# Kernel tuning notes

Measured on AMD Instinct MI355X. Metric: run time of the kernel, lower is better.

Reference implementation:

```python
import jax, jax.numpy as jnp
import numpy as np
import math

B, N, E, H = 2, 10000, 160000, 128
ET = 8
EPS = 1e-5


def setup_inputs() -> dict:
    key = jax.random.key(0)
    ks = jax.random.split(key, 20)
    s = 1.0 / math.sqrt(H)
    inp = {
        "hidden": jax.random.normal(ks[0], (B, N, H), jnp.float32),
        "time_emb": jax.random.normal(ks[1], (B, N, H), jnp.float32),
        "edge_index": jax.random.randint(ks[2], (2, E), 0, N),
        "edge_type": jax.random.randint(ks[3], (E,), 0, ET),
        # parameters
        "edge_emb": jax.random.normal(ks[4], (ET, H), jnp.float32),
        "Wq": jax.random.normal(ks[5], (H, H), jnp.float32) * s,
        "bq": jnp.zeros((H,), jnp.float32),
        "Wk": jax.random.normal(ks[6], (H, H), jnp.float32) * s,
        "bk": jnp.zeros((H,), jnp.float32),
        "Wv": jax.random.normal(ks[7], (H, H), jnp.float32) * s,
        "bv": jnp.zeros((H,), jnp.float32),
        "We": jax.random.normal(ks[8], (H, 1), jnp.float32) * s,
        "be": jnp.zeros((1,), jnp.float32),
        "W1": jax.random.normal(ks[9], (3 * H, H), jnp.float32) * (1.0 / math.sqrt(3 * H)),
        "b1": jnp.zeros((H,), jnp.float32),
        "W2": jax.random.normal(ks[10], (H, H), jnp.float32) * s,
        "b2": jnp.zeros((H,), jnp.float32),
        "gamma": jnp.ones((H,), jnp.float32),
        "beta": jnp.zeros((H,), jnp.float32),
    }
    return inp


def _forward(hidden, time_emb, edge_index, edge_type, edge_emb,
             Wq, bq, Wk, bk, Wv, bv, We, be, W1, b1, W2, b2, gamma, beta):
    src, tgt = edge_index[0], edge_index[1]
    # edge-wise gathers: [B, E, H]
    src_h = hidden[:, src]
    tgt_h = hidden[:, tgt]
    src_t = time_emb[:, src]
    tgt_t = time_emb[:, tgt]
    edge_h = edge_emb[edge_type][None, :, :]  # [1, E, H] broadcasts over batch

    query = (tgt_h + tgt_t) @ Wq + bq
    key = (src_h + src_t + edge_h) @ Wk + bk
    value = (src_h + edge_h) @ Wv + bv

    logits = jnp.einsum("beh,beh->be", query, key) / math.sqrt(H)
    logits = logits + (edge_h @ We + be)[..., 0]  # edge bias broadcast over batch

    # segment softmax per target node (equivalent to the per-node masked softmax loop)
    lT = logits.T  # [E, B]
    seg_max = jax.ops.segment_max(lT, tgt, num_segments=N)          # [N, B]
    seg_max = jnp.where(jnp.isfinite(seg_max), seg_max, 0.0)
    ex = jnp.exp(lT - seg_max[tgt])                                  # [E, B]
    seg_sum = jax.ops.segment_sum(ex, tgt, num_segments=N)           # [N, B]
    weights = (ex / seg_sum[tgt]).T                                  # [B, E]

    messages = value * weights[..., None]                            # [B, E, H]
    # scatter-add to target nodes
    agg = jax.ops.segment_sum(jnp.swapaxes(messages, 0, 1), tgt, num_segments=N)  # [N, B, H]
    aggregated = jnp.swapaxes(agg, 0, 1)                             # [B, N, H]

    cat = jnp.concatenate([hidden, aggregated, time_emb], axis=-1)   # [B, N, 3H]
    updated = jax.nn.silu(cat @ W1 + b1) @ W2 + b2

    x = hidden + updated  # dropout p=0 -> identity
    mu = jnp.mean(x, axis=-1, keepdims=True)
    var = jnp.var(x, axis=-1, keepdims=True)
    return (x - mu) * jax.lax.rsqrt(var + EPS) * gamma + beta


def reference(hidden, time_emb, edge_index, edge_type, edge_emb,
              Wq, bq, Wk, bk, Wv, bv, We, be, W1, b1, W2, b2, gamma, beta):
    return _forward(hidden, time_emb, edge_index, edge_type, edge_emb,
                    Wq, bq, Wk, bk, Wv, bv, We, be, W1, b1, W2, b2, gamma, beta)
```

## Files before the change

kernel.cpp:

```cpp
#include <hip/hip_runtime.h>
#include <math.h>

constexpr int B_  = 2;
constexpr int N_  = 10000;
constexpr int E_  = 160000;
constexpr int H_  = 128;
constexpr int ET_ = 8;
constexpr float EPS_ = 1e-5f;
constexpr float RSQH = 0.08838834764831845f;

typedef __bf16 bf16x8 __attribute__((ext_vector_type(8)));
typedef short  short8 __attribute__((ext_vector_type(8)));
typedef float  f32x4  __attribute__((ext_vector_type(4)));
typedef unsigned short u16;

__device__ inline u16 bf16b(float f) {
    return __builtin_bit_cast(u16, (__bf16)f);
}

__global__ __launch_bounds__(512)
void prep_w_kernel(const float* __restrict__ W1, const float* __restrict__ W2,
                   const float* __restrict__ Wq, const float* __restrict__ Wk,
                   const float* __restrict__ Wv,
                   u16* __restrict__ W1s, u16* __restrict__ W2s,
                   u16* __restrict__ Wqs, u16* __restrict__ Wks,
                   u16* __restrict__ Wvs)
{
    int bid = blockIdx.x;
    const float* src; u16* dst; int kc;
    if (bid < 12)      { src = W1; dst = W1s; kc = bid; }
    else if (bid < 16) { src = W2; dst = W2s; kc = bid - 12; }
    else if (bid < 20) { src = Wq; dst = Wqs; kc = bid - 16; }
    else if (bid < 24) { src = Wk; dst = Wks; kc = bid - 20; }
    else               { src = Wv; dst = Wvs; kc = bid - 24; }
    int nt = threadIdx.x >> 6, lane = threadIdx.x & 63;
    int q = lane >> 4, c = lane & 15;
    int kbase = kc * 32 + q * 8;
    int col = nt * 16 + c;
    u16* out = dst + ((kc * 8 + nt) * 64 + lane) * 8;
#pragma unroll
    for (int j = 0; j < 8; ++j)
        out[j] = bf16b(src[(kbase + j) * H_ + col]);
}

__device__ inline bf16x8 ldfrag(const u16* __restrict__ W, int kc, int nt, int lane) {
    short8 s = *(const short8*)(W + ((kc * 8 + nt) * 64 + lane) * 8);
    return __builtin_bit_cast(bf16x8, s);
}

__global__ __launch_bounds__(256)
void qkv_mfma_kernel(const float* __restrict__ hidden, const float* __restrict__ time_emb,
                     const u16* __restrict__ Wqs, const u16* __restrict__ Wks,
                     const u16* __restrict__ Wvs, const float* __restrict__ bq,
                     u16* __restrict__ Q, u16* __restrict__ K, u16* __restrict__ V)
{
    const int wv = threadIdx.x >> 6, lane = threadIdx.x & 63;
    const int tile = blockIdx.x * 4 + wv;
    if (tile >= (B_ * N_) / 16) return;
    const int nbase = tile * 16;
    const int m = lane & 15, q = lane >> 4;
    const int koff = q * 8;

    bf16x8 aq[4], av[4];
    const float* hp = hidden   + (nbase + m) * H_ + koff;
    const float* tp = time_emb + (nbase + m) * H_ + koff;
#pragma unroll
    for (int kc = 0; kc < 4; ++kc) {
        float4 h0 = *(const float4*)(hp + kc * 32);
        float4 h1 = *(const float4*)(hp + kc * 32 + 4);
        float4 t0 = *(const float4*)(tp + kc * 32);
        float4 t1 = *(const float4*)(tp + kc * 32 + 4);
        bf16x8 fv, fq;
        fv[0]=(__bf16)h0.x; fv[1]=(__bf16)h0.y; fv[2]=(__bf16)h0.z; fv[3]=(__bf16)h0.w;
        fv[4]=(__bf16)h1.x; fv[5]=(__bf16)h1.y; fv[6]=(__bf16)h1.z; fv[7]=(__bf16)h1.w;
        fq[0]=(__bf16)(h0.x+t0.x); fq[1]=(__bf16)(h0.y+t0.y);
        fq[2]=(__bf16)(h0.z+t0.z); fq[3]=(__bf16)(h0.w+t0.w);
        fq[4]=(__bf16)(h1.x+t1.x); fq[5]=(__bf16)(h1.y+t1.y);
        fq[6]=(__bf16)(h1.z+t1.z); fq[7]=(__bf16)(h1.w+t1.w);
        av[kc] = fv; aq[kc] = fq;
    }

    f32x4 accq[8], acck[8], accv[8];
#pragma unroll
    for (int nt = 0; nt < 8; ++nt) { accq[nt] = (f32x4)0.f; acck[nt] = (f32x4)0.f; accv[nt] = (f32x4)0.f; }

#pragma unroll
    for (int kc = 0; kc < 4; ++kc) {
#pragma unroll
        for (int nt = 0; nt < 8; ++nt) {
            bf16x8 bfq = ldfrag(Wqs, kc, nt, lane);
            bf16x8 bfk = ldfrag(Wks, kc, nt, lane);
            bf16x8 bfv = ldfrag(Wvs, kc, nt, lane);
            accq[nt] = __builtin_amdgcn_mfma_f32_16x16x32_bf16(aq[kc], bfq, accq[nt], 0, 0, 0);
            acck[nt] = __builtin_amdgcn_mfma_f32_16x16x32_bf16(aq[kc], bfk, acck[nt], 0, 0, 0);
            accv[nt] = __builtin_amdgcn_mfma_f32_16x16x32_bf16(av[kc], bfv, accv[nt], 0, 0, 0);
        }
    }

#pragma unroll
    for (int nt = 0; nt < 8; ++nt) {
        int col = nt * 16 + m;
        float bqc = bq[col];
#pragma unroll
        for (int r = 0; r < 4; ++r) {
            int node = nbase + q * 4 + r;
            Q[node * H_ + col] = bf16b(accq[nt][r] + bqc);
            K[node * H_ + col] = bf16b(acck[nt][r]);
            V[node * H_ + col] = bf16b(accv[nt][r]);
        }
    }
}

__global__ __launch_bounds__(128)
void edgetab_kernel(const float* __restrict__ edge_emb,
                    const float* __restrict__ Wk, const float* __restrict__ bk,
                    const float* __restrict__ Wv, const float* __restrict__ bv,
                    const float* __restrict__ We, const float* __restrict__ be,
                    float* __restrict__ Kt, float* __restrict__ Vt, float* __restrict__ eb)
{
    const int t = blockIdx.x, j = threadIdx.x;
    const float* ep = edge_emb + t * H_;
    float ak = bk[j], av = bv[j];
    for (int d = 0; d < H_; d += 4) {
        float e0 = ep[d], e1 = ep[d+1], e2 = ep[d+2], e3 = ep[d+3];
        ak += e0*Wk[(d+0)*H_+j] + e1*Wk[(d+1)*H_+j] + e2*Wk[(d+2)*H_+j] + e3*Wk[(d+3)*H_+j];
        av += e0*Wv[(d+0)*H_+j] + e1*Wv[(d+1)*H_+j] + e2*Wv[(d+2)*H_+j] + e3*Wv[(d+3)*H_+j];
    }
    Kt[t*H_ + j] = ak;
    Vt[t*H_ + j] = av;

    __shared__ float red[2];
    float pe = ep[j] * We[j];
#pragma unroll
    for (int off = 32; off; off >>= 1) pe += __shfl_xor(pe, off);
    if ((j & 63) == 0) red[j >> 6] = pe;
    __syncthreads();
    if (j == 0) eb[t] = red[0] + red[1] + be[0];
}

__global__ void hist_kernel(const int* __restrict__ tgt, int* __restrict__ hist)
{
    int e = blockIdx.x * blockDim.x + threadIdx.x;
    if (e < E_) atomicAdd(&hist[tgt[e]], 1);
}

__global__ __launch_bounds__(1024)
void scan_kernel(const int* __restrict__ hist, int* __restrict__ offs, int* __restrict__ cursor)
{
    __shared__ int wpart[16];
    __shared__ int wexcl[16];
    __shared__ int carry_s;
    const int tid = threadIdx.x, wave = tid >> 6, lane = tid & 63;
    if (tid == 0) carry_s = 0;
    __syncthreads();
    for (int base = 0; base < N_; base += 1024) {
        int idx = base + tid;
        int v = (idx < N_) ? hist[idx] : 0;
        int s = v;
#pragma unroll
        for (int off = 1; off < 64; off <<= 1) {
            int t = __shfl_up(s, off);
            if (lane >= off) s += t;
        }
        if (lane == 63) wpart[wave] = s;
        __syncthreads();
        if (tid == 0) {
            int c = carry_s;
            for (int w = 0; w < 16; ++w) { int p = wpart[w]; wexcl[w] = c; c += p; }
            carry_s = c;
        }
        __syncthreads();
        if (idx < N_) {
            int excl = wexcl[wave] + s - v;
            offs[idx] = excl;
            cursor[idx] = excl;
        }
        __syncthreads();
    }
    if (threadIdx.x == 0) offs[N_] = carry_s;
}

__global__ void scatter_kernel(const int* __restrict__ src, const int* __restrict__ tgt,
                               const int* __restrict__ type, int* __restrict__ cursor,
                               int* __restrict__ sorted)
{
    int e = blockIdx.x * blockDim.x + threadIdx.x;
    if (e < E_) {
        int t = tgt[e];
        int pos = atomicAdd(&cursor[t], 1);
        sorted[pos] = src[e] | (type[e] << 16);
    }
}

__global__ __launch_bounds__(256)
void attn_kernel(const u16* __restrict__ Qb, const u16* __restrict__ Kb,
                 const u16* __restrict__ Vb,
                 const float* __restrict__ Kt, const float* __restrict__ Vt,
                 const float* __restrict__ eb,
                 const int* __restrict__ offs, const int* __restrict__ sorted,
                 u16* __restrict__ aggb)
{
    __shared__ float logit_s[4][64];
    __shared__ float bias_s[4][8];
    __shared__ __align__(16) u16 vt_s[8][128];

    const int tid = threadIdx.x;
    const int wv = tid >> 6, lane = tid & 63;
    const int g = lane >> 4, lam = lane & 15;

    for (int idx = tid; idx < ET_ * H_; idx += 256)
        vt_s[idx >> 7][idx & 127] = bf16b(Vt[idx]);
    __syncthreads();

    const int b = blockIdx.x & 1;
    const int n = (blockIdx.x >> 1) * 4 + wv;
    const int bn = b * N_ + n;
    const int beg = offs[n], end = offs[n + 1];
    const int bbase = b * N_;

    float q[8];
    {
        short8 s8 = *(const short8*)(Qb + (size_t)bn * H_ + lam * 8);
        bf16x8 qa = __builtin_bit_cast(bf16x8, s8);
#pragma unroll
        for (int j = 0; j < 8; ++j) q[j] = (float)qa[j];
    }

    {
        const float* k0p = Kt + (2 * g) * H_ + lam * 8;
        const float* k1p = Kt + (2 * g + 1) * H_ + lam * 8;
        float p0 = 0.f, p1 = 0.f;
#pragma unroll
        for (int j = 0; j < 8; ++j) { p0 += q[j] * k0p[j]; p1 += q[j] * k1p[j]; }
#pragma unroll
        for (int msk = 1; msk < 16; msk <<= 1) {
            p0 += __shfl_xor(p0, msk);
            p1 += __shfl_xor(p1, msk);
        }
        if (lam == 0) {
            bias_s[wv][2 * g]     = p0 * RSQH + eb[2 * g];
            bias_s[wv][2 * g + 1] = p1 * RSQH + eb[2 * g + 1];
        }
    }

    float m_run = -INFINITY, l = 0.f;
    float acc[8];
#pragma unroll
    for (int j = 0; j < 8; ++j) acc[j] = 0.f;

    for (int cb = beg; cb < end; cb += 64) {
        const int cnt = min(64, end - cb);
        float gmax = -INFINITY;
        for (int c = g; c < cnt; c += 4) {
            int pk = sorted[cb + c];
            int s = pk & 0xFFFF, t = pk >> 16;
            short8 k8 = *(const short8*)(Kb + (size_t)(bbase + s) * H_ + lam * 8);
            bf16x8 ka = __builtin_bit_cast(bf16x8, k8);
            float p = 0.f;
#pragma unroll
            for (int j = 0; j < 8; ++j) p += q[j] * (float)ka[j];
#pragma unroll
            for (int msk = 1; msk < 16; msk <<= 1) p += __shfl_xor(p, msk);
            float lg = p * RSQH + bias_s[wv][t];
            if (lam == 0) logit_s[wv][c] = lg;
            gmax = fmaxf(gmax, lg);
        }
        gmax = fmaxf(gmax, __shfl_xor(gmax, 16));
        gmax = fmaxf(gmax, __shfl_xor(gmax, 32));
        float Mn = fmaxf(m_run, gmax);
        float rs = __expf(m_run - Mn);
        l *= rs;
#pragma unroll
        for (int j = 0; j < 8; ++j) acc[j] *= rs;
        m_run = Mn;
        for (int c = g; c < cnt; c += 4) {
            int pk = sorted[cb + c];
            int s = pk & 0xFFFF, t = pk >> 16;
            float w = __expf(logit_s[wv][c] - Mn);
            l += w;
            short8 v8  = *(const short8*)(Vb + (size_t)(bbase + s) * H_ + lam * 8);
            short8 vt8 = *(const short8*)(&vt_s[t][lam * 8]);
            bf16x8 va  = __builtin_bit_cast(bf16x8, v8);
            bf16x8 vta = __builtin_bit_cast(bf16x8, vt8);
#pragma unroll
            for (int j = 0; j < 8; ++j)
                acc[j] += w * ((float)va[j] + (float)vta[j]);
        }
    }

#pragma unroll
    for (int j = 0; j < 8; ++j) {
        acc[j] += __shfl_xor(acc[j], 16);
        acc[j] += __shfl_xor(acc[j], 32);
    }
    l += __shfl_xor(l, 16);
    l += __shfl_xor(l, 32);

    if (g == 0) {
        float invL = (end > beg) ? 1.f / l : 0.f;
        bf16x8 o;
#pragma unroll
        for (int j = 0; j < 8; ++j) o[j] = (__bf16)(acc[j] * invL);
        *(short8*)(aggb + (size_t)bn * H_ + lam * 8) = __builtin_bit_cast(short8, o);
    }
}

__global__ __launch_bounds__(256)
void mlp_mfma_kernel(const float* __restrict__ hidden, const u16* __restrict__ aggb,
                     const float* __restrict__ time_emb,
                     const u16* __restrict__ W1s, const u16* __restrict__ W2s,
                     const float* __restrict__ b1, const float* __restrict__ b2,
                     const float* __restrict__ gamma, const float* __restrict__ beta,
                     float* __restrict__ out)
{
    __shared__ __align__(16) u16 h1s[4][16][136];
    const int wv = threadIdx.x >> 6, lane = threadIdx.x & 63;
    const int tile = blockIdx.x * 4 + wv;
    if (tile >= (B_ * N_) / 16) return;
    const int nbase = tile * 16;
    const int m = lane & 15, q = lane >> 4;
    const int koff = q * 8;

    bf16x8 a[12];
    const float* hp = hidden   + (nbase + m) * H_ + koff;
    const float* tp = time_emb + (nbase + m) * H_ + koff;
    const u16*   ap = aggb + (size_t)(nbase + m) * H_ + koff;
#pragma unroll
    for (int kc = 0; kc < 4; ++kc) {
        float4 h0 = *(const float4*)(hp + kc * 32);
        float4 h1 = *(const float4*)(hp + kc * 32 + 4);
        float4 t0 = *(const float4*)(tp + kc * 32);
        float4 t1 = *(const float4*)(tp + kc * 32 + 4);
        bf16x8 fh, ft;
        fh[0]=(__bf16)h0.x; fh[1]=(__bf16)h0.y; fh[2]=(__bf16)h0.z; fh[3]=(__bf16)h0.w;
        fh[4]=(__bf16)h1.x; fh[5]=(__bf16)h1.y; fh[6]=(__bf16)h1.z; fh[7]=(__bf16)h1.w;
        ft[0]=(__bf16)t0.x; ft[1]=(__bf16)t0.y; ft[2]=(__bf16)t0.z; ft[3]=(__bf16)t0.w;
        ft[4]=(__bf16)t1.x; ft[5]=(__bf16)t1.y; ft[6]=(__bf16)t1.z; ft[7]=(__bf16)t1.w;
        a[0 * 4 + kc] = fh;
        a[2 * 4 + kc] = ft;
        short8 s8 = *(const short8*)(ap + kc * 32);
        a[1 * 4 + kc] = __builtin_bit_cast(bf16x8, s8);
    }

    f32x4 acc[8];
#pragma unroll
    for (int nt = 0; nt < 8; ++nt) acc[nt] = (f32x4)0.f;
#pragma unroll
    for (int kc = 0; kc < 12; ++kc) {
#pragma unroll
        for (int nt = 0; nt < 8; ++nt) {
            bf16x8 bf = ldfrag(W1s, kc, nt, lane);
            acc[nt] = __builtin_amdgcn_mfma_f32_16x16x32_bf16(a[kc], bf, acc[nt], 0, 0, 0);
        }
    }

#pragma unroll
    for (int nt = 0; nt < 8; ++nt) {
        int col = nt * 16 + m;
        float bb = b1[col];
#pragma unroll
        for (int r = 0; r < 4; ++r) {
            float v = acc[nt][r] + bb;
            float h = v / (1.f + __expf(-v));
            h1s[wv][q * 4 + r][col] = bf16b(h);
        }
    }

    f32x4 acc2[8];
#pragma unroll
    for (int nt = 0; nt < 8; ++nt) acc2[nt] = (f32x4)0.f;
#pragma unroll
    for (int kc = 0; kc < 4; ++kc) {
        short8 s8 = *(const short8*)&h1s[wv][m][kc * 32 + koff];
        bf16x8 a2 = __builtin_bit_cast(bf16x8, s8);
#pragma unroll
        for (int nt = 0; nt < 8; ++nt) {
            bf16x8 bf = ldfrag(W2s, kc, nt, lane);
            acc2[nt] = __builtin_amdgcn_mfma_f32_16x16x32_bf16(a2, bf, acc2[nt], 0, 0, 0);
        }
    }

    float x[8][4];
#pragma unroll
    for (int nt = 0; nt < 8; ++nt) {
        int col = nt * 16 + m;
        float bb = b2[col];
#pragma unroll
        for (int r = 0; r < 4; ++r) {
            int node = nbase + q * 4 + r;
            x[nt][r] = hidden[node * H_ + col] + acc2[nt][r] + bb;
        }
    }
#pragma unroll
    for (int r = 0; r < 4; ++r) {
        float s = 0.f, ss = 0.f;
#pragma unroll
        for (int nt = 0; nt < 8; ++nt) { s += x[nt][r]; ss += x[nt][r] * x[nt][r]; }
#pragma unroll
        for (int off = 1; off < 16; off <<= 1) {
            s  += __shfl_xor(s, off);
            ss += __shfl_xor(ss, off);
        }
        float mu  = s * (1.f / H_);
        float var = ss * (1.f / H_) - mu * mu;
        float rs  = rsqrtf(var + EPS_);
        int node = nbase + q * 4 + r;
#pragma unroll
        for (int nt = 0; nt < 8; ++nt) {
            int col = nt * 16 + m;
            out[node * H_ + col] = (x[nt][r] - mu) * rs * gamma[col] + beta[col];
        }
    }
}

extern "C" void kernel_launch(void* const* d_in, const int* in_sizes, int n_in,
                              void* d_out, int out_size, void* d_ws, size_t ws_size,
                              hipStream_t stream)
{
    const float* hidden   = (const float*)d_in[0];
    const float* time_emb = (const float*)d_in[1];
    const int*   eidx     = (const int*)d_in[2];
    const int*   etype    = (const int*)d_in[3];
    const float* edge_emb = (const float*)d_in[4];
    const float* Wq = (const float*)d_in[5];
    const float* bq = (const float*)d_in[6];
    const float* Wk = (const float*)d_in[7];
    const float* bk = (const float*)d_in[8];
    const float* Wv = (const float*)d_in[9];
    const float* bv = (const float*)d_in[10];
    const float* We = (const float*)d_in[11];
    const float* be = (const float*)d_in[12];
    const float* W1 = (const float*)d_in[13];
    const float* b1 = (const float*)d_in[14];
    const float* W2 = (const float*)d_in[15];
    const float* b2 = (const float*)d_in[16];
    const float* gamma = (const float*)d_in[17];
    const float* beta  = (const float*)d_in[18];
    float* out = (float*)d_out;

    constexpr int BNH = B_ * N_ * H_;
    u16* Qb   = (u16*)d_ws;
    u16* Kb   = Qb + BNH;
    u16* Vb   = Kb + BNH;
    u16* aggb = Vb + BNH;
    float* Kt  = (float*)(aggb + BNH);
    float* Vt  = Kt + ET_ * H_;
    float* ebt = Vt + ET_ * H_;
    int* hist   = (int*)(ebt + ET_);
    int* offs   = hist + N_;
    int* cursor = offs + (N_ + 1);
    int* sorted = cursor + N_;
    uintptr_t wp = (uintptr_t)(sorted + E_);
    wp = (wp + 15) & ~(uintptr_t)15;
    u16* W1s = (u16*)wp;
    u16* W2s = W1s + 384 * 128;
    u16* Wqs = W2s + 128 * 128;
    u16* Wks = Wqs + 128 * 128;
    u16* Wvs = Wks + 128 * 128;

    const int* esrc = eidx;
    const int* etgt = eidx + E_;

    hipMemsetAsync(hist, 0, N_ * sizeof(int), stream);

    prep_w_kernel<<<28, 512, 0, stream>>>(W1, W2, Wq, Wk, Wv, W1s, W2s, Wqs, Wks, Wvs);
    qkv_mfma_kernel<<<313, 256, 0, stream>>>(hidden, time_emb, Wqs, Wks, Wvs, bq, Qb, Kb, Vb);
    edgetab_kernel<<<ET_, 128, 0, stream>>>(edge_emb, Wk, bk, Wv, bv, We, be, Kt, Vt, ebt);
    hist_kernel<<<(E_ + 255) / 256, 256, 0, stream>>>(etgt, hist);
    scan_kernel<<<1, 1024, 0, stream>>>(hist, offs, cursor);
    scatter_kernel<<<(E_ + 255) / 256, 256, 0, stream>>>(esrc, etgt, etype, cursor, sorted);
    attn_kernel<<<(B_ * N_) / 4, 256, 0, stream>>>(Qb, Kb, Vb, Kt, Vt, ebt, offs, sorted, aggb);
    mlp_mfma_kernel<<<313, 256, 0, stream>>>(hidden, aggb, time_emb, W1s, W2s, b1, b2, gamma, beta, out);
}
```

Baseline: 212.6 us.

## Merge setup kernels, parallelize scan, fuse scatter with QKV, unroll attention loops

Combines weight prep, edge-type table and histogram into one launch, rewrites the scan so each thread handles 10 elements with no serial loop, and runs the CSR scatter and the QKV GEMM as one launch using block-index ranges. The attention kernel now stages the packed edge indices in shared memory once per chunk and processes two edges per iteration, giving more memory-level parallelism on the K/V gathers. This cuts launch overhead and serial scan time, at the cost of heterogeneous blocks sharing one launch configuration and higher register pressure in attention.

```diff
diff --git a/kernel.cpp b/kernel.cpp
--- a/kernel.cpp
+++ b/kernel.cpp
@@ -18,44 +18,131 @@
     return __builtin_bit_cast(u16, (__bf16)f);
 }
 
-__global__ __launch_bounds__(512)
-void prep_w_kernel(const float* __restrict__ W1, const float* __restrict__ W2,
-                   const float* __restrict__ Wq, const float* __restrict__ Wk,
-                   const float* __restrict__ Wv,
-                   u16* __restrict__ W1s, u16* __restrict__ W2s,
-                   u16* __restrict__ Wqs, u16* __restrict__ Wks,
-                   u16* __restrict__ Wvs)
-{
-    int bid = blockIdx.x;
-    const float* src; u16* dst; int kc;
-    if (bid < 12)      { src = W1; dst = W1s; kc = bid; }
-    else if (bid < 16) { src = W2; dst = W2s; kc = bid - 12; }
-    else if (bid < 20) { src = Wq; dst = Wqs; kc = bid - 16; }
-    else if (bid < 24) { src = Wk; dst = Wks; kc = bid - 20; }
-    else               { src = Wv; dst = Wvs; kc = bid - 24; }
-    int nt = threadIdx.x >> 6, lane = threadIdx.x & 63;
-    int q = lane >> 4, c = lane & 15;
-    int kbase = kc * 32 + q * 8;
-    int col = nt * 16 + c;
-    u16* out = dst + ((kc * 8 + nt) * 64 + lane) * 8;
-#pragma unroll
-    for (int j = 0; j < 8; ++j)
-        out[j] = bf16b(src[(kbase + j) * H_ + col]);
-}
-
 __device__ inline bf16x8 ldfrag(const u16* __restrict__ W, int kc, int nt, int lane) {
     short8 s = *(const short8*)(W + ((kc * 8 + nt) * 64 + lane) * 8);
     return __builtin_bit_cast(bf16x8, s);
 }
 
 __global__ __launch_bounds__(256)
-void qkv_mfma_kernel(const float* __restrict__ hidden, const float* __restrict__ time_emb,
-                     const u16* __restrict__ Wqs, const u16* __restrict__ Wks,
-                     const u16* __restrict__ Wvs, const float* __restrict__ bq,
-                     u16* __restrict__ Q, u16* __restrict__ K, u16* __restrict__ V)
+void setup_kernel(const float* __restrict__ W1, const float* __restrict__ W2,
+                  const float* __restrict__ Wq, const float* __restrict__ Wk,
+                  const float* __restrict__ Wv,
+                  u16* __restrict__ W1s, u16* __restrict__ W2s,
+                  u16* __restrict__ Wqs, u16* __restrict__ Wks, u16* __restrict__ Wvs,
+                  const float* __restrict__ edge_emb,
+                  const float* __restrict__ bk, const float* __restrict__ bv,
+                  const float* __restrict__ We, const float* __restrict__ be,
+                  float* __restrict__ Kt, float* __restrict__ Vt, float* __restrict__ eb,
+                  const int* __restrict__ tgt, int* __restrict__ hist)
 {
+    const int bid = blockIdx.x, tid = threadIdx.x;
+    if (bid < 56) {
+        int unit = bid >> 1, half = bid & 1;
+        const float* src; u16* dst; int kc;
+        if (unit < 12)      { src = W1; dst = W1s; kc = unit; }
+        else if (unit < 16) { src = W2; dst = W2s; kc = unit - 12; }
+        else if (unit < 20) { src = Wq; dst = Wqs; kc = unit - 16; }
+        else if (unit < 24) { src = Wk; dst = Wks; kc = unit - 20; }
+        else                { src = Wv; dst = Wvs; kc = unit - 24; }
+        int nt = half * 4 + (tid >> 6), lane = tid & 63;
+        int q = lane >> 4, c = lane & 15;
+        int kbase = kc * 32 + q * 8;
+        int col = nt * 16 + c;
+        u16* out = dst + ((kc * 8 + nt) * 64 + lane) * 8;
+#pragma unroll
+        for (int j = 0; j < 8; ++j)
+            out[j] = bf16b(src[(kbase + j) * H_ + col]);
+    } else if (bid < 64) {
+        int t = bid - 56;
+        const float* ep = edge_emb + t * H_;
+        __shared__ float red[2];
+        int j = tid;
+        if (j < 128) {
+            float ak = bk[j], av = bv[j];
+            for (int d = 0; d < H_; d += 4) {
+                float e0 = ep[d], e1 = ep[d+1], e2 = ep[d+2], e3 = ep[d+3];
+                ak += e0*Wk[(d+0)*H_+j] + e1*Wk[(d+1)*H_+j] + e2*Wk[(d+2)*H_+j] + e3*Wk[(d+3)*H_+j];
+                av += e0*Wv[(d+0)*H_+j] + e1*Wv[(d+1)*H_+j] + e2*Wv[(d+2)*H_+j] + e3*Wv[(d+3)*H_+j];
+            }
+            Kt[t*H_ + j] = ak;
+            Vt[t*H_ + j] = av;
+            float pe = ep[j] * We[j];
+#pragma unroll
+            for (int off = 32; off; off >>= 1) pe += __shfl_xor(pe, off);
+            if ((j & 63) == 0) red[j >> 6] = pe;
+        }
+        __syncthreads();
+        if (j == 0) eb[t] = red[0] + red[1] + be[0];
+    } else {
+        int e = (bid - 64) * 256 + tid;
+        if (e < E_) atomicAdd(&hist[tgt[e]], 1);
+    }
+}
+
+__global__ __launch_bounds__(1024)
+void scan_kernel(const int* __restrict__ hist, int* __restrict__ offs,
+                 int* __restrict__ cursor)
+{
+    __shared__ int winc[16];
+    const int tid = threadIdx.x, wave = tid >> 6, lane = tid & 63;
+    int v[10];
+    const int idx0 = tid * 10;
+    int tot = 0;
+#pragma unroll
+    for (int i = 0; i < 10; ++i) {
+        int idx = idx0 + i;
+        v[i] = (idx < N_) ? hist[idx] : 0;
+        tot += v[i];
+    }
+    int s = tot;
+#pragma unroll
+    for (int off = 1; off < 64; off <<= 1) {
+        int t = __shfl_up(s, off);
+        if (lane >= off) s += t;
+    }
+    if (lane == 63) winc[wave] = s;
+    __syncthreads();
+    if (tid < 16) {
+        int si = winc[tid];
+#pragma unroll
+        for (int off = 1; off < 16; off <<= 1) {
+            int t = __shfl_up(si, off);
+            if (tid >= off) si += t;
+        }
+        winc[tid] = si;
+    }
+    __syncthreads();
+    int wbase = (wave == 0) ? 0 : winc[wave - 1];
+    int run = wbase + (s - tot);
+#pragma unroll
+    for (int i = 0; i < 10; ++i) {
+        int idx = idx0 + i;
+        if (idx < N_) { offs[idx] = run; cursor[idx] = run; }
+        run += v[i];
+    }
+    if (tid == 0) offs[N_] = winc[15];
+}
+
+__global__ __launch_bounds__(256)
+void scatter_qkv_kernel(const int* __restrict__ src, const int* __restrict__ tgt,
+                        const int* __restrict__ type, int* __restrict__ cursor,
+                        int* __restrict__ sorted,
+                        const float* __restrict__ hidden, const float* __restrict__ time_emb,
+                        const u16* __restrict__ Wqs, const u16* __restrict__ Wks,
+                        const u16* __restrict__ Wvs, const float* __restrict__ bq,
+                        u16* __restrict__ Q, u16* __restrict__ K, u16* __restrict__ V)
+{
+    if (blockIdx.x < 625) {
+        int e = blockIdx.x * 256 + threadIdx.x;
+        if (e < E_) {
+            int t = tgt[e];
+            int pos = atomicAdd(&cursor[t], 1);
+            sorted[pos] = src[e] | (type[e] << 16);
+        }
+        return;
+    }
     const int wv = threadIdx.x >> 6, lane = threadIdx.x & 63;
-    const int tile = blockIdx.x * 4 + wv;
+    const int tile = (blockIdx.x - 625) * 4 + wv;
     if (tile >= (B_ * N_) / 16) return;
     const int nbase = tile * 16;
     const int m = lane & 15, q = lane >> 4;
@@ -111,87 +198,6 @@
     }
 }
 
-__global__ __launch_bounds__(128)
-void edgetab_kernel(const float* __restrict__ edge_emb,
-                    const float* __restrict__ Wk, const float* __restrict__ bk,
-                    const float* __restrict__ Wv, const float* __restrict__ bv,
-                    const float* __restrict__ We, const float* __restrict__ be,
-                    float* __restrict__ Kt, float* __restrict__ Vt, float* __restrict__ eb)
-{
-    const int t = blockIdx.x, j = threadIdx.x;
-    const float* ep = edge_emb + t * H_;
-    float ak = bk[j], av = bv[j];
-    for (int d = 0; d < H_; d += 4) {
-        float e0 = ep[d], e1 = ep[d+1], e2 = ep[d+2], e3 = ep[d+3];
-        ak += e0*Wk[(d+0)*H_+j] + e1*Wk[(d+1)*H_+j] + e2*Wk[(d+2)*H_+j] + e3*Wk[(d+3)*H_+j];
-        av += e0*Wv[(d+0)*H_+j] + e1*Wv[(d+1)*H_+j] + e2*Wv[(d+2)*H_+j] + e3*Wv[(d+3)*H_+j];
-    }
-    Kt[t*H_ + j] = ak;
-    Vt[t*H_ + j] = av;
-
-    __shared__ float red[2];
-    float pe = ep[j] * We[j];
-#pragma unroll
-    for (int off = 32; off; off >>= 1) pe += __shfl_xor(pe, off);
-    if ((j & 63) == 0) red[j >> 6] = pe;
-    __syncthreads();
-    if (j == 0) eb[t] = red[0] + red[1] + be[0];
-}
-
-__global__ void hist_kernel(const int* __restrict__ tgt, int* __restrict__ hist)
-{
-    int e = blockIdx.x * blockDim.x + threadIdx.x;
-    if (e < E_) atomicAdd(&hist[tgt[e]], 1);
-}
-
-__global__ __launch_bounds__(1024)
-void scan_kernel(const int* __restrict__ hist, int* __restrict__ offs, int* __restrict__ cursor)
-{
-    __shared__ int wpart[16];
-    __shared__ int wexcl[16];
-    __shared__ int carry_s;
-    const int tid = threadIdx.x, wave = tid >> 6, lane = tid & 63;
-    if (tid == 0) carry_s = 0;
-    __syncthreads();
-    for (int base = 0; base < N_; base += 1024) {
-        int idx = base + tid;
-        int v = (idx < N_) ? hist[idx] : 0;
-        int s = v;
-#pragma unroll
-        for (int off = 1; off < 64; off <<= 1) {
-            int t = __shfl_up(s, off);
-            if (lane >= off) s += t;
-        }
-        if (lane == 63) wpart[wave] = s;
-        __syncthreads();
-        if (tid == 0) {
-            int c = carry_s;
-            for (int w = 0; w < 16; ++w) { int p = wpart[w]; wexcl[w] = c; c += p; }
-            carry_s = c;
-        }
-        __syncthreads();
-        if (idx < N_) {
-            int excl = wexcl[wave] + s - v;
-            offs[idx] = excl;
-            cursor[idx] = excl;
-        }
-        __syncthreads();
-    }
-    if (threadIdx.x == 0) offs[N_] = carry_s;
-}
-
-__global__ void scatter_kernel(const int* __restrict__ src, const int* __restrict__ tgt,
-                               const int* __restrict__ type, int* __restrict__ cursor,
-                               int* __restrict__ sorted)
-{
-    int e = blockIdx.x * blockDim.x + threadIdx.x;
-    if (e < E_) {
-        int t = tgt[e];
-        int pos = atomicAdd(&cursor[t], 1);
-        sorted[pos] = src[e] | (type[e] << 16);
-    }
-}
-
 __global__ __launch_bounds__(256)
 void attn_kernel(const u16* __restrict__ Qb, const u16* __restrict__ Kb,
                  const u16* __restrict__ Vb,
@@ -202,6 +208,7 @@
 {
     __shared__ float logit_s[4][64];
     __shared__ float bias_s[4][8];
+    __shared__ int   pk_s[4][64];
     __shared__ __align__(16) u16 vt_s[8][128];
 
     const int tid = threadIdx.x;
@@ -250,20 +257,48 @@
 
     for (int cb = beg; cb < end; cb += 64) {
         const int cnt = min(64, end - cb);
+        pk_s[wv][lane] = (cb + lane < end) ? sorted[cb + lane] : 0;
+
         float gmax = -INFINITY;
-        for (int c = g; c < cnt; c += 4) {
-            int pk = sorted[cb + c];
-            int s = pk & 0xFFFF, t = pk >> 16;
-            short8 k8 = *(const short8*)(Kb + (size_t)(bbase + s) * H_ + lam * 8);
-            bf16x8 ka = __builtin_bit_cast(bf16x8, k8);
-            float p = 0.f;
-#pragma unroll
-            for (int j = 0; j < 8; ++j) p += q[j] * (float)ka[j];
-#pragma unroll
-            for (int msk = 1; msk < 16; msk <<= 1) p += __shfl_xor(p, msk);
-            float lg = p * RSQH + bias_s[wv][t];
-            if (lam == 0) logit_s[wv][c] = lg;
-            gmax = fmaxf(gmax, lg);
+        int c = g;
+        for (; c + 4 < cnt; c += 8) {
+            int pk0 = pk_s[wv][c];
+            int pk1 = pk_s[wv][c + 4];
+            int s0 = pk0 & 0xFFFF, t0 = pk0 >> 16;
+            int s1 = pk1 & 0xFFFF, t1 = pk1 >> 16;
+            short8 k80 = *(const short8*)(Kb + (size_t)(bbase + s0) * H_ + lam * 8);
+            short8 k81 = *(const short8*)(Kb + (size_t)(bbase + s1) * H_ + lam * 8);
+            bf16x8 ka0 = __builtin_bit_cast(bf16x8, k80);
+            bf16x8 ka1 = __builtin_bit_cast(bf16x8, k81);
+            float p0 = 0.f, p1 = 0.f;
+#pragma unroll
+            for (int j = 0; j < 8; ++j) {
+                p0 += q[j] * (float)ka0[j];
+                p1 += q[j] * (float)ka1[j];
+            }
+#pragma unroll
+            for (int msk = 1; msk < 16; msk <<= 1) {
+                p0 += __shfl_xor(p0, msk);
+                p1 += __shfl_xor(p1, msk);
+            }
+            float lg0 = p0 * RSQH + bias_s[wv][t0];
+            float lg1 = p1 * RSQH + bias_s[wv][t1];
+            if (lam == 0) { logit_s[wv][c] = lg0; logit_s[wv][c + 4] = lg1; }
+            gmax = fmaxf(gmax, fmaxf(lg0, lg1));
+        }
+        if (c < cnt) {
+            int pk0 = pk_s[wv][c];
+            int s0 = pk0 & 0xFFFF, t0 = pk0 >> 16;
+            short8 k80 = *(const short8*)(Kb + (size_t)(bbase + s0) * H_ + lam * 8);
+            bf16x8 ka0 = __builtin_bit_cast(bf16x8, k80);
+            float p0 = 0.f;
+#pragma unroll
+            for (int j = 0; j < 8; ++j) p0 += q[j] * (float)ka0[j];
+#pragma unroll
+            for (int msk = 1; msk < 16; msk <<= 1) p0 += __shfl_xor(p0, msk);
+            float lg0 = p0 * RSQH + bias_s[wv][t0];
+            if (lam == 0) logit_s[wv][c] = lg0;
+            gmax = fmaxf(gmax, lg0);
         }
         gmax = fmaxf(gmax, __shfl_xor(gmax, 16));
         gmax = fmaxf(gmax, __shfl_xor(gmax, 32));
@@ -273,18 +308,41 @@
 #pragma unroll
         for (int j = 0; j < 8; ++j) acc[j] *= rs;
         m_run = Mn;
-        for (int c = g; c < cnt; c += 4) {
-            int pk = sorted[cb + c];
-            int s = pk & 0xFFFF, t = pk >> 16;
-            float w = __expf(logit_s[wv][c] - Mn);
-            l += w;
-            short8 v8  = *(const short8*)(Vb + (size_t)(bbase + s) * H_ + lam * 8);
-            short8 vt8 = *(const short8*)(&vt_s[t][lam * 8]);
-            bf16x8 va  = __builtin_bit_cast(bf16x8, v8);
-            bf16x8 vta = __builtin_bit_cast(bf16x8, vt8);
+
+        c = g;
+        for (; c + 4 < cnt; c += 8) {
+            int pk0 = pk_s[wv][c];
+            int pk1 = pk_s[wv][c + 4];
+            int s0 = pk0 & 0xFFFF, t0 = pk0 >> 16;
+            int s1 = pk1 & 0xFFFF, t1 = pk1 >> 16;
+            short8 v80  = *(const short8*)(Vb + (size_t)(bbase + s0) * H_ + lam * 8);
+            short8 v81  = *(const short8*)(Vb + (size_t)(bbase + s1) * H_ + lam * 8);
+            short8 vt80 = *(const short8*)(&vt_s[t0][lam * 8]);
+            short8 vt81 = *(const short8*)(&vt_s[t1][lam * 8]);
+            float w0 = __expf(logit_s[wv][c] - Mn);
+            float w1 = __expf(logit_s[wv][c + 4] - Mn);
+            l += w0 + w1;
+            bf16x8 va0  = __builtin_bit_cast(bf16x8, v80);
+            bf16x8 va1  = __builtin_bit_cast(bf16x8, v81);
+            bf16x8 vta0 = __builtin_bit_cast(bf16x8, vt80);
+            bf16x8 vta1 = __builtin_bit_cast(bf16x8, vt81);
 #pragma unroll
             for (int j = 0; j < 8; ++j)
-                acc[j] += w * ((float)va[j] + (float)vta[j]);
+                acc[j] += w0 * ((float)va0[j] + (float)vta0[j])
+                        + w1 * ((float)va1[j] + (float)vta1[j]);
+        }
+        if (c < cnt) {
+            int pk0 = pk_s[wv][c];
+            int s0 = pk0 & 0xFFFF, t0 = pk0 >> 16;
+            short8 v80  = *(const short8*)(Vb + (size_t)(bbase + s0) * H_ + lam * 8);
+            short8 vt80 = *(const short8*)(&vt_s[t0][lam * 8]);
+            float w0 = __expf(logit_s[wv][c] - Mn);
+            l += w0;
+            bf16x8 va0  = __builtin_bit_cast(bf16x8, v80);
+            bf16x8 vta0 = __builtin_bit_cast(bf16x8, vt80);
+#pragma unroll
+            for (int j = 0; j < 8; ++j)
+                acc[j] += w0 * ((float)va0[j] + (float)vta0[j]);
         }
     }
 
@@ -463,12 +521,13 @@
 
     hipMemsetAsync(hist, 0, N_ * sizeof(int), stream);
 
-    prep_w_kernel<<<28, 512, 0, stream>>>(W1, W2, Wq, Wk, Wv, W1s, W2s, Wqs, Wks, Wvs);
-    qkv_mfma_kernel<<<313, 256, 0, stream>>>(hidden, time_emb, Wqs, Wks, Wvs, bq, Qb, Kb, Vb);
-    edgetab_kernel<<<ET_, 128, 0, stream>>>(edge_emb, Wk, bk, Wv, bv, We, be, Kt, Vt, ebt);
-    hist_kernel<<<(E_ + 255) / 256, 256, 0, stream>>>(etgt, hist);
+    setup_kernel<<<64 + (E_ + 255) / 256, 256, 0, stream>>>(
+        W1, W2, Wq, Wk, Wv, W1s, W2s, Wqs, Wks, Wvs,
+        edge_emb, bk, bv, We, be, Kt, Vt, ebt, etgt, hist);
     scan_kernel<<<1, 1024, 0, stream>>>(hist, offs, cursor);
-    scatter_kernel<<<(E_ + 255) / 256, 256, 0, stream>>>(esrc, etgt, etype, cursor, sorted);
+    scatter_qkv_kernel<<<625 + 313, 256, 0, stream>>>(
+        esrc, etgt, etype, cursor, sorted,
+        hidden, time_emb, Wqs, Wks, Wvs, bq, Qb, Kb, Vb);
     attn_kernel<<<(B_ * N_) / 4, 256, 0, stream>>>(Qb, Kb, Vb, Kt, Vt, ebt, offs, sorted, aggb);
     mlp_mfma_kernel<<<313, 256, 0, stream>>>(hidden, aggb, time_emb, W1s, W2s, b1, b2, gamma, beta, out);
 }
```

Result: faster. 195.7 us (median of 2 runs) (-7.9%).
